# Performance work log

Measured on AMD Instinct MI355X. Metric: run time of the kernel, lower is better.

## Reference

```python
import jax, jax.numpy as jnp
import numpy as np

B, N, D, H = 1, 4096, 1024, 16
K = D // H
ROPE_BASE = 10000.0


def _rope_cos_sin(n, k, base, dtype):
    # GPT-NeoX style rotary embedding: inv_freq over even dims, emb = cat(freqs, freqs)
    inv_freq = 1.0 / (base ** (jnp.arange(0, k, 2, dtype=jnp.float32) / k))  # [K/2]
    pos = jnp.arange(n, dtype=jnp.float32)
    freqs = pos[:, None] * inv_freq[None, :]              # [N, K/2]
    emb = jnp.concatenate([freqs, freqs], axis=-1)        # [N, K]
    return jnp.cos(emb).astype(dtype), jnp.sin(emb).astype(dtype)


def _rotate_half(x):
    x1, x2 = jnp.split(x, 2, axis=-1)
    return jnp.concatenate([-x2, x1], axis=-1)


def setup_inputs() -> dict:
    key = jax.random.key(0)
    kx, kq, ko = jax.random.split(key, 3)
    x = jax.random.normal(kx, (B, N, D), dtype=jnp.float32)
    # torch Linear weights: [out_features, in_features], y = x @ W^T
    w_qkv = jax.random.normal(kq, (3 * H * K, D), dtype=jnp.float32) / np.sqrt(D)
    w_out = jax.random.normal(ko, (D, D), dtype=jnp.float32) / np.sqrt(D)
    return {"x": x, "w_qkv": w_qkv, "w_out": w_out}


def reference(x, w_qkv, w_out):
    b, n, d = x.shape
    qkv = jnp.einsum('bnd,ed->bne', x, w_qkv).reshape(b, n, 3, H, K)
    q, k, v = qkv[:, :, 0], qkv[:, :, 1], qkv[:, :, 2]   # [B, N, H, K]
    cos, sin = _rope_cos_sin(n, K, ROPE_BASE, x.dtype)    # [N, K]
    cos = cos[None, :, None, :]
    sin = sin[None, :, None, :]
    q = q * cos + _rotate_half(q) * sin
    k = k * cos + _rotate_half(k) * sin
    # explicit O(N^2) score matrix, as in the original module
    scores = jnp.einsum('bnhk,bmhk->bnhm', q, k) / np.sqrt(K).astype(x.dtype)
    causal_mask = jnp.tril(jnp.ones((n, n), dtype=bool))  # [N, M]
    scores = jnp.where(causal_mask[None, :, None, :], scores, jnp.finfo(x.dtype).min)
    probs = jax.nn.softmax(scores, axis=-1)
    attn = jnp.einsum('bnhm,bmhk->bnhk', probs, v).reshape(b, n, d)
    return jnp.einsum('bnd,ed->bne', attn, w_out)
```

## Files before the change

kernel.cpp:

```cpp
#include <hip/hip_runtime.h>
#include <hip/hip_bf16.h>
#include <math.h>

#define N_SEQ 4096
#define DIM   1024
#define NHEAD 16
#define HDIM  64
#define E3    3072

typedef short bf16x8 __attribute__((ext_vector_type(8)));
typedef float f32x4  __attribute__((ext_vector_type(4)));
typedef unsigned int u32;

#if __has_builtin(__builtin_amdgcn_exp2f)
#define EXP2(x) __builtin_amdgcn_exp2f(x)
#else
#define EXP2(x) exp2f(x)
#endif

__device__ __forceinline__ float bf2f(unsigned short u) {
    union { unsigned int i; float f; } x; x.i = ((unsigned int)u) << 16; return x.f;
}
__device__ __forceinline__ unsigned short f2bf(float f) {
    union { float f; unsigned int i; } x; x.f = f;
    unsigned int r = x.i + 0x7FFF + ((x.i >> 16) & 1);
    return (unsigned short)(r >> 16);
}
__device__ __forceinline__ unsigned short f2bf_fast(float f) {
    union { float f; unsigned int i; } x; x.f = f;
    return (unsigned short)((x.i + 0x8000u) >> 16);
}
__device__ __forceinline__ f32x4 mfma16(bf16x8 a, bf16x8 b, f32x4 c) {
    return __builtin_amdgcn_mfma_f32_16x16x32_bf16(a, b, c, 0, 0, 0);
}
__device__ __forceinline__ void gload_lds16(const unsigned short* g, unsigned short* l) {
    __builtin_amdgcn_global_load_lds(
        (const __attribute__((address_space(1))) u32*)g,
        (__attribute__((address_space(3))) u32*)l, 16, 0, 0);
}

__device__ __forceinline__ int probe_isf32(const unsigned short* __restrict__ X) {
    __shared__ int cnt;
    if (threadIdx.x == 0) cnt = 0;
    __syncthreads();
    int bad = 0;
    for (int i = threadIdx.x; i < 4096; i += 256) {
        float v = bf2f(X[i]);
        if (!(fabsf(v) < 1e10f)) bad = 1;
    }
    if (bad) atomicAdd(&cnt, 1);
    __syncthreads();
    return cnt > 0;
}

__global__ __launch_bounds__(256)
void prep_kernel(const void* __restrict__ X, const void* __restrict__ Wq,
                 const void* __restrict__ Wo,
                 unsigned short* __restrict__ Xb, unsigned short* __restrict__ Wqb,
                 unsigned short* __restrict__ Wob,
                 float4* __restrict__ Rt,
                 int* __restrict__ flag)
{
    const int ti = blockIdx.x * blockDim.x + threadIdx.x;
    if (ti < N_SEQ * 16) {
        const int n = ti >> 4, f = ti & 15;
        const float i0 = powf(10000.f, -((float)f)        * (1.f/32.f));
        const float i1 = powf(10000.f, -((float)(f + 16)) * (1.f/32.f));
        float s0, c0, s1, c1;
        sincosf((float)n * i0, &s0, &c0);
        sincosf((float)n * i1, &s1, &c1);
        Rt[ti] = (float4){c0, c1, s0, s1};
    }

    const int isf32 = probe_isf32((const unsigned short*)X);
    if (blockIdx.x == 0 && threadIdx.x == 0) *flag = isf32;
    if (!isf32) return;

    const int nX4  = (N_SEQ * DIM) >> 2;
    const int nWq4 = (E3 * DIM) >> 2;
    const int nWo4 = (DIM * DIM) >> 2;
    const int total = nX4 + nWq4 + nWo4;
    const int stride = gridDim.x * blockDim.x;
    for (int i = blockIdx.x * blockDim.x + threadIdx.x; i < total; i += stride) {
        const float4* src; ushort4* dst; int j = i;
        if (j < nX4)                { src = (const float4*)X  + j;  dst = (ushort4*)Xb  + j; }
        else if ((j -= nX4) < nWq4) { src = (const float4*)Wq + j;  dst = (ushort4*)Wqb + j; }
        else { j -= nWq4;             src = (const float4*)Wo + j;  dst = (ushort4*)Wob + j; }
        float4 v = *src;
        ushort4 u;
        u.x = f2bf(v.x); u.y = f2bf(v.y); u.z = f2bf(v.z); u.w = f2bf(v.w);
        *dst = u;
    }
}

__global__ __launch_bounds__(256)
void qkv_mfma_kernel(const void* __restrict__ Xo, const unsigned short* __restrict__ Xc,
                     const void* __restrict__ Wo_, const unsigned short* __restrict__ Wc,
                     const int* __restrict__ flag,
                     const float4* __restrict__ Rt,
                     unsigned short* __restrict__ Qf,
                     unsigned short* __restrict__ Kf,
                     unsigned short* __restrict__ Vf)
{
    __shared__ __align__(16) unsigned short SMEM[4][4096];

    const int isf32 = *flag;
    const unsigned short* Xb = isf32 ? Xc : (const unsigned short*)Xo;
    const unsigned short* Wb = isf32 ? Wc : (const unsigned short*)Wo_;

    const int tid  = threadIdx.x;
    const int lane = tid & 63;
    const int wave = tid >> 6;
    const int wr = wave >> 1, wc = wave & 1;
    const int lm = lane & 15, q4 = lane >> 4;
    const int rbase = blockIdx.y * 128;
    const int cbase = blockIdx.x * 128;

    const int srow = wave * 16 + (lane >> 2);
    const int scol = (lane & 3) * 8;

    const unsigned short* xsrc = Xb + (size_t)(rbase + srow) * DIM + scol;
    const unsigned short* wsrc = Wb + (size_t)(cbase + srow) * DIM + scol;
    const int la = (wr*64 + lm)*32 + q4*8;
    const int lb = (wc*64 + lm)*32 + q4*8;

    f32x4 acc[4][4];
    #pragma unroll
    for (int i = 0; i < 4; ++i)
        #pragma unroll
        for (int j = 0; j < 4; ++j) acc[i][j] = (f32x4){0.f, 0.f, 0.f, 0.f};

    #define QSTAGE(buf)                                                             \
        {                                                                           \
            _Pragma("unroll")                                                       \
            for (int j = 0; j < 2; ++j) {                                           \
                gload_lds16(xsrc + (size_t)j*64*DIM, &SMEM[buf][j*2048 + wave*512]);   \
                gload_lds16(wsrc + (size_t)j*64*DIM, &SMEM[2+buf][j*2048 + wave*512]); \
            }                                                                       \
            xsrc += 32; wsrc += 32;                                                 \
        }

    QSTAGE(0)
    for (int it = 0; it < DIM/32; ++it) {
        const int cur = it & 1;
        __syncthreads();
        if (it + 1 < DIM/32) QSTAGE(cur ^ 1)

        bf16x8 a[4], b[4];
        #pragma unroll
        for (int mi = 0; mi < 4; ++mi)
            a[mi] = *(const bf16x8*)&SMEM[cur][la + mi*512];
        #pragma unroll
        for (int ni = 0; ni < 4; ++ni)
            b[ni] = *(const bf16x8*)&SMEM[2+cur][lb + ni*512];
        #pragma unroll
        for (int mi = 0; mi < 4; ++mi)
            #pragma unroll
            for (int ni = 0; ni < 4; ++ni)
                acc[mi][ni] = mfma16(a[mi], b[ni], acc[mi][ni]);
    }
    #undef QSTAGE

    __syncthreads();

    const int ecol = cbase + wc * 64;
    const int part = ecol >> 10;
    const int h    = (ecol >> 6) & 15;
    unsigned short* ep = &SMEM[0][0] + wave*4096;

    if (part == 2) {
        #pragma unroll
        for (int mh = 0; mh < 2; ++mh) {
            #pragma unroll
            for (int mi2 = 0; mi2 < 2; ++mi2) {
                const int mi = mh*2 + mi2;
                #pragma unroll
                for (int r = 0; r < 4; ++r) {
                    const int n31 = mi2*16 + q4*4 + r;
                    #pragma unroll
                    for (int ni = 0; ni < 4; ++ni)
                        ep[(ni*16 + lm)*40 + n31] = f2bf(acc[mi][ni][r]);
                }
            }
            const int nb = rbase + wr*64 + mh*32;
            const size_t vb = (((size_t)h*128 + (nb >> 5)) << 11) + (size_t)lane*8;
            #pragma unroll
            for (int ni = 0; ni < 4; ++ni) {
                const bf16x8 fr = *(const bf16x8*)(ep + (ni*16 + lm)*40 + q4*8);
                *(bf16x8*)(Vf + vb + (size_t)ni*512) = fr;
            }
        }
    } else {
        unsigned short* dst = (part == 0) ? Qf : Kf;
        const float scl = (part == 0) ? 0.180336884f : 1.0f;
        #pragma unroll
        for (int mi = 0; mi < 4; ++mi) {
            const int tn = rbase + wr*64 + mi*16;
            #pragma unroll
            for (int r = 0; r < 4; ++r) {
                const int n = tn + q4*4 + r;
                const float4 t = Rt[(n << 4) + lm];
                const int row = (q4*4 + r)*72;
                ep[row + lm]      = f2bf((acc[mi][0][r]*t.x - acc[mi][2][r]*t.z) * scl);
                ep[row + lm + 16] = f2bf((acc[mi][1][r]*t.y - acc[mi][3][r]*t.w) * scl);
                ep[row + lm + 32] = f2bf((acc[mi][2][r]*t.x + acc[mi][0][r]*t.z) * scl);
                ep[row + lm + 48] = f2bf((acc[mi][3][r]*t.y + acc[mi][1][r]*t.w) * scl);
            }
            const size_t tb = (((size_t)(h*256 + (tn >> 4))) << 10) + (size_t)lane*8;
            #pragma unroll
            for (int c = 0; c < 2; ++c) {
                const bf16x8 fr = *(const bf16x8*)(ep + lm*72 + c*32 + q4*8);
                *(bf16x8*)(dst + tb + (size_t)c*512) = fr;
            }
        }
    }
}

__global__ __launch_bounds__(512, 4)
void attn_mfma_kernel(const unsigned short* __restrict__ Qf,
                      const unsigned short* __restrict__ Kf,
                      const unsigned short* __restrict__ Vf,
                      unsigned short* __restrict__ Attn)
{
    __shared__ __align__(16) unsigned short P16[8][2][16][40];
    __shared__ __align__(16) float Ox[4][16][64];
    __shared__ float Lx[4][16];

    const int tid  = threadIdx.x;
    const int lane = tid & 63;
    const int wave = tid >> 6;
    const int q4 = lane >> 4, lm = lane & 15;
    const int qh = wave >> 1;
    const int kh = wave & 1;

    const int h = blockIdx.x & 15;
    const int p = blockIdx.x >> 4;
    const int qwA = (p << 6) + (qh << 4);
    const int qwB = ((63 - p) << 6) + (qh << 4);
    const int ntA = p + 1;
    const int ntB = 64 - p;

    const unsigned short* qpA = Qf + (((size_t)(h*256 + (qwA >> 4))) << 10) + (size_t)lane * 8;
    const unsigned short* qpB = Qf + (((size_t)(h*256 + (qwB >> 4))) << 10) + (size_t)lane * 8;
    bf16x8 aqA[2], aqB[2];
    #pragma unroll
    for (int d = 0; d < 2; ++d) {
        aqA[d] = *(const bf16x8*)(qpA + d*512);
        aqB[d] = *(const bf16x8*)(qpB + d*512);
    }

    float lA[4], lB[4];
    f32x4 oA[4], oB[4];
    #pragma unroll
    for (int r = 0; r < 4; ++r) { lA[r] = 0.f; lB[r] = 0.f; }
    #pragma unroll
    for (int dc = 0; dc < 4; ++dc) {
        oA[dc] = (f32x4){0.f, 0.f, 0.f, 0.f};
        oB[dc] = (f32x4){0.f, 0.f, 0.f, 0.f};
    }

    const size_t hb = ((size_t)h) << 18;
    const unsigned short* kc = Kf + hb + (size_t)(kh*2048) + (size_t)lane*8;
    const unsigned short* vc = Vf + hb + (size_t)(kh*2048) + (size_t)lane*8;

    unsigned short* pwA  = &P16[wave][0][0][0];
    unsigned short* pwB  = &P16[wave][1][0][0];
    unsigned short* pwaA = pwA + (4*q4)*40 + lm;
    unsigned short* pwaB = pwB + (4*q4)*40 + lm;
    const unsigned short* parA = pwA + lm*40 + q4*8;
    const unsigned short* parB = pwB + lm*40 + q4*8;

    bf16x8 bk[2][2];
    bk[0][0] = *(const bf16x8*)(kc);
    bk[0][1] = *(const bf16x8*)(kc + 512);
    bk[1][0] = *(const bf16x8*)(kc + 1024);
    bk[1][1] = *(const bf16x8*)(kc + 1536);

    for (int it = 0; it < ntB; ++it) {
        const int kt = it << 6;
        const int doA = (it < ntA);

        bf16x8 bv[4];
        #pragma unroll
        for (int dc = 0; dc < 4; ++dc)
            bv[dc] = *(const bf16x8*)(vc + dc*512);

        bf16x8 nk[2][2];
        nk[0][0] = *(const bf16x8*)(kc + 4096);
        nk[0][1] = *(const bf16x8*)(kc + 4096 + 512);
        nk[1][0] = *(const bf16x8*)(kc + 4096 + 1024);
        nk[1][1] = *(const bf16x8*)(kc + 4096 + 1536);

        f32x4 sB[2], sA[2];
        #pragma unroll
        for (int ki = 0; ki < 2; ++ki) {
            f32x4 z = (f32x4){0.f, 0.f, 0.f, 0.f};
            z = mfma16(aqB[0], bk[ki][0], z);
            sB[ki] = mfma16(aqB[1], bk[ki][1], z);
        }
        if (doA) {
            #pragma unroll
            for (int ki = 0; ki < 2; ++ki) {
                f32x4 z = (f32x4){0.f, 0.f, 0.f, 0.f};
                z = mfma16(aqA[0], bk[ki][0], z);
                sA[ki] = mfma16(aqA[1], bk[ki][1], z);
            }
        }

        if (kt + 32*kh + 31 > qwB) {
            #pragma unroll
            for (int ki = 0; ki < 2; ++ki) {
                const int key = kt + 32*kh + 16*ki + lm;
                const int qq = qwB + 4*q4;
                #pragma unroll
                for (int r = 0; r < 4; ++r)
                    if (key > qq + r) sB[ki][r] = -INFINITY;
            }
        }

        #pragma unroll
        for (int ki = 0; ki < 2; ++ki)
            #pragma unroll
            for (int r = 0; r < 4; ++r) {
                const float pb = EXP2(sB[ki][r]);
                lB[r] += pb;
                pwaB[r*40 + ki*16] = f2bf_fast(pb);
            }

        if (doA) {
            if (kt + 32*kh + 31 > qwA) {
                #pragma unroll
                for (int ki = 0; ki < 2; ++ki) {
                    const int key = kt + 32*kh + 16*ki + lm;
                    const int qq = qwA + 4*q4;
                    #pragma unroll
                    for (int r = 0; r < 4; ++r)
                        if (key > qq + r) sA[ki][r] = -INFINITY;
                }
            }
            #pragma unroll
            for (int ki = 0; ki < 2; ++ki)
                #pragma unroll
                for (int r = 0; r < 4; ++r) {
                    const float pa = EXP2(sA[ki][r]);
                    lA[r] += pa;
                    pwaA[r*40 + ki*16] = f2bf_fast(pa);
                }
        }

        {
            const bf16x8 paB = *(const bf16x8*)(parB);
            #pragma unroll
            for (int dc = 0; dc < 4; ++dc)
                oB[dc] = mfma16(paB, bv[dc], oB[dc]);
        }
        if (doA) {
            const bf16x8 paA = *(const bf16x8*)(parA);
            #pragma unroll
            for (int dc = 0; dc < 4; ++dc)
                oA[dc] = mfma16(paA, bv[dc], oA[dc]);
        }

        kc += 4096; vc += 4096;
        bk[0][0] = nk[0][0]; bk[0][1] = nk[0][1];
        bk[1][0] = nk[1][0]; bk[1][1] = nk[1][1];
    }

    #pragma unroll
    for (int r = 0; r < 4; ++r) {
        float a = lA[r], b = lB[r];
        #pragma unroll
        for (int mk = 1; mk <= 8; mk <<= 1) {
            a += __shfl_xor(a, mk);
            b += __shfl_xor(b, mk);
        }
        lA[r] = a; lB[r] = b;
    }

    if (kh == 1) {
        #pragma unroll
        for (int r = 0; r < 4; ++r) {
            const int qq = 4*q4 + r;
            #pragma unroll
            for (int dc = 0; dc < 4; ++dc)
                Ox[qh][qq][16*dc + lm] = oA[dc][r];
            if (lm == 0) Lx[qh][qq] = lA[r];
        }
    }
    __syncthreads();
    if (kh == 0) {
        #pragma unroll
        for (int r = 0; r < 4; ++r) {
            const int qq = 4*q4 + r;
            const float inv = 1.f / (lA[r] + Lx[qh][qq]);
            const size_t row = (size_t)(qwA + qq) * DIM + (h << 6) + lm;
            #pragma unroll
            for (int dc = 0; dc < 4; ++dc) {
                const float v = oA[dc][r] + Ox[qh][qq][16*dc + lm];
                Attn[row + 16*dc] = f2bf(v * inv);
            }
        }
    }
    __syncthreads();
    if (kh == 1) {
        #pragma unroll
        for (int r = 0; r < 4; ++r) {
            const int qq = 4*q4 + r;
            #pragma unroll
            for (int dc = 0; dc < 4; ++dc)
                Ox[qh][qq][16*dc + lm] = oB[dc][r];
            if (lm == 0) Lx[qh][qq] = lB[r];
        }
    }
    __syncthreads();
    if (kh == 0) {
        #pragma unroll
        for (int r = 0; r < 4; ++r) {
            const int qq = 4*q4 + r;
            const float inv = 1.f / (lB[r] + Lx[qh][qq]);
            const size_t row = (size_t)(qwB + qq) * DIM + (h << 6) + lm;
            #pragma unroll
            for (int dc = 0; dc < 4; ++dc) {
                const float v = oB[dc][r] + Ox[qh][qq][16*dc + lm];
                Attn[row + 16*dc] = f2bf(v * inv);
            }
        }
    }
}

__global__ __launch_bounds__(256)
void out_mfma_kernel(const unsigned short* __restrict__ Ab,
                     const void* __restrict__ Wo_, const unsigned short* __restrict__ Wc,
                     const int* __restrict__ flag,
                     void* __restrict__ Out)
{
    __shared__ unsigned short As[2][4096];
    __shared__ unsigned short Bs[2][2048];

    const int isf32 = *flag;
    const unsigned short* Wb = isf32 ? Wc : (const unsigned short*)Wo_;

    const int tid  = threadIdx.x;
    const int lane = tid & 63;
    const int wave = tid >> 6;
    const int lm = lane & 15, q4 = lane >> 4;
    const int rbase = blockIdx.y * 128;
    const int cbase = blockIdx.x * 64;

    const int srow16 = lane >> 2;
    const int scol = (lane & 3) * 8;

    const unsigned short* asrc = Ab + (size_t)(rbase + wave*32 + srow16) * DIM + scol;
    const unsigned short* bsrc = Wb + (size_t)(cbase + wave*16 + srow16) * DIM + scol;
    const int la = (wave*32 + lm)*32 + q4*8;
    const int lb = lm*32 + q4*8;

    f32x4 acc[2][4];
    #pragma unroll
    for (int i = 0; i < 2; ++i)
        #pragma unroll
        for (int j = 0; j < 4; ++j) acc[i][j] = (f32x4){0.f, 0.f, 0.f, 0.f};

    #define OSTAGE(buf)                                                          \
        {                                                                        \
            _Pragma("unroll")                                                    \
            for (int j = 0; j < 2; ++j)                                          \
                gload_lds16(asrc + (size_t)j*16*DIM, &As[buf][(wave*32 + j*16)*32]); \
            gload_lds16(bsrc, &Bs[buf][(wave*16)*32]);                           \
            asrc += 32; bsrc += 32;                                              \
        }

    OSTAGE(0)
    for (int it = 0; it < DIM/32; ++it) {
        const int cur = it & 1;
        __syncthreads();
        if (it + 1 < DIM/32) OSTAGE(cur ^ 1)

        bf16x8 a[2], b[4];
        #pragma unroll
        for (int mi = 0; mi < 2; ++mi)
            a[mi] = *(const bf16x8*)&As[cur][la + mi*512];
        #pragma unroll
        for (int ni = 0; ni < 4; ++ni)
            b[ni] = *(const bf16x8*)&Bs[cur][lb + ni*512];
        #pragma unroll
        for (int mi = 0; mi < 2; ++mi)
            #pragma unroll
            for (int ni = 0; ni < 4; ++ni)
                acc[mi][ni] = mfma16(a[mi], b[ni], acc[mi][ni]);
    }
    #undef OSTAGE

    #pragma unroll
    for (int mi = 0; mi < 2; ++mi)
        #pragma unroll
        for (int r = 0; r < 4; ++r) {
            const size_t n = rbase + wave*32 + mi*16 + q4*4 + r;
            #pragma unroll
            for (int ni = 0; ni < 4; ++ni) {
                const size_t e = cbase + ni*16 + lm;
                const float v = acc[mi][ni][r];
                if (isf32) ((float*)Out)[n * DIM + e] = v;
                else       ((unsigned short*)Out)[n * DIM + e] = f2bf(v);
            }
        }
}

extern "C" void kernel_launch(void* const* d_in, const int* in_sizes, int n_in,
                              void* d_out, int out_size, void* d_ws, size_t ws_size,
                              hipStream_t stream) {
    const void* X    = d_in[0];
    const void* Wqkv = d_in[1];
    const void* Wout = d_in[2];

    int* flag = (int*)d_ws;
    unsigned short* base = (unsigned short*)((char*)d_ws + 256);
    const size_t nX = (size_t)N_SEQ * DIM;
    const size_t nWq = (size_t)E3 * DIM;
    const size_t nWo = (size_t)DIM * DIM;
    unsigned short* Xb  = base;
    unsigned short* Wqb = Xb + nX;
    unsigned short* Wob = Wqb + nWq;
    unsigned short* Qf  = Wob + nWo;
    unsigned short* Kf  = Qf + nX;
    unsigned short* Vf  = Kf + nX;
    unsigned short* At  = Vf + nX;
    float4* Rt = (float4*)(At + nX);

    prep_kernel<<<768, 256, 0, stream>>>(X, Wqkv, Wout, Xb, Wqb, Wob, Rt, flag);
    qkv_mfma_kernel<<<dim3(E3 / 128, N_SEQ / 128), 256, 0, stream>>>(X, Xb, Wqkv, Wqb, flag, Rt, Qf, Kf, Vf);
    attn_mfma_kernel<<<dim3(NHEAD * 32), 512, 0, stream>>>(Qf, Kf, Vf, At);
    out_mfma_kernel<<<dim3(DIM / 64, N_SEQ / 128), 256, 0, stream>>>(At, Wout, Wob, flag, d_out);
}
```

Baseline: 223.6 us.

## Process four query tiles per attention block to reuse K/V loads

```diff
diff --git a/kernel.cpp b/kernel.cpp
--- a/kernel.cpp
+++ b/kernel.cpp
@@ -216,13 +216,13 @@
     }
 }
 
-__global__ __launch_bounds__(512, 4)
+__global__ __launch_bounds__(512, 2)
 void attn_mfma_kernel(const unsigned short* __restrict__ Qf,
                       const unsigned short* __restrict__ Kf,
                       const unsigned short* __restrict__ Vf,
                       unsigned short* __restrict__ Attn)
 {
-    __shared__ __align__(16) unsigned short P16[8][2][16][40];
+    __shared__ __align__(16) unsigned short P16[8][4][16][40];
     __shared__ __align__(16) float Ox[4][16][64];
     __shared__ float Lx[4][16];
 
@@ -235,40 +235,42 @@
 
     const int h = blockIdx.x & 15;
     const int p = blockIdx.x >> 4;
-    const int qwA = (p << 6) + (qh << 4);
-    const int qwB = ((63 - p) << 6) + (qh << 4);
-    const int ntA = p + 1;
-    const int ntB = 64 - p;
-
-    const unsigned short* qpA = Qf + (((size_t)(h*256 + (qwA >> 4))) << 10) + (size_t)lane * 8;
-    const unsigned short* qpB = Qf + (((size_t)(h*256 + (qwB >> 4))) << 10) + (size_t)lane * 8;
-    bf16x8 aqA[2], aqB[2];
-    #pragma unroll
-    for (int d = 0; d < 2; ++d) {
-        aqA[d] = *(const bf16x8*)(qpA + d*512);
-        aqB[d] = *(const bf16x8*)(qpB + d*512);
-    }
-
-    float lA[4], lB[4];
-    f32x4 oA[4], oB[4];
-    #pragma unroll
-    for (int r = 0; r < 4; ++r) { lA[r] = 0.f; lB[r] = 0.f; }
-    #pragma unroll
-    for (int dc = 0; dc < 4; ++dc) {
-        oA[dc] = (f32x4){0.f, 0.f, 0.f, 0.f};
-        oB[dc] = (f32x4){0.f, 0.f, 0.f, 0.f};
+
+    int qb[4], nt[4], qw[4];
+    qb[0] = 63 - p; qb[1] = 32 + p; qb[2] = 31 - p; qb[3] = p;
+    #pragma unroll
+    for (int s = 0; s < 4; ++s) { nt[s] = qb[s] + 1; qw[s] = qb[s]*64 + qh*16; }
+
+    bf16x8 aq[4][2];
+    #pragma unroll
+    for (int s = 0; s < 4; ++s) {
+        const unsigned short* qp = Qf + (((size_t)(h*256 + (qw[s] >> 4))) << 10) + (size_t)lane * 8;
+        aq[s][0] = *(const bf16x8*)(qp);
+        aq[s][1] = *(const bf16x8*)(qp + 512);
+    }
+
+    float l[4][4];
+    f32x4 o[4][4];
+    #pragma unroll
+    for (int s = 0; s < 4; ++s) {
+        #pragma unroll
+        for (int r = 0; r < 4; ++r) l[s][r] = 0.f;
+        #pragma unroll
+        for (int dc = 0; dc < 4; ++dc) o[s][dc] = (f32x4){0.f, 0.f, 0.f, 0.f};
     }
 
     const size_t hb = ((size_t)h) << 18;
     const unsigned short* kc = Kf + hb + (size_t)(kh*2048) + (size_t)lane*8;
     const unsigned short* vc = Vf + hb + (size_t)(kh*2048) + (size_t)lane*8;
 
-    unsigned short* pwA  = &P16[wave][0][0][0];
-    unsigned short* pwB  = &P16[wave][1][0][0];
-    unsigned short* pwaA = pwA + (4*q4)*40 + lm;
-    unsigned short* pwaB = pwB + (4*q4)*40 + lm;
-    const unsigned short* parA = pwA + lm*40 + q4*8;
-    const unsigned short* parB = pwB + lm*40 + q4*8;
+    unsigned short* pwa[4];
+    const unsigned short* par[4];
+    #pragma unroll
+    for (int s = 0; s < 4; ++s) {
+        unsigned short* base = &P16[wave][s][0][0];
+        pwa[s] = base + (4*q4)*40 + lm;
+        par[s] = base + lm*40 + q4*8;
+    }
 
     bf16x8 bk[2][2];
     bk[0][0] = *(const bf16x8*)(kc);
@@ -276,9 +278,9 @@
     bk[1][0] = *(const bf16x8*)(kc + 1024);
     bk[1][1] = *(const bf16x8*)(kc + 1536);
 
-    for (int it = 0; it < ntB; ++it) {
+    const int ntmax = nt[0];
+    for (int it = 0; it < ntmax; ++it) {
         const int kt = it << 6;
-        const int doA = (it < ntA);
 
         bf16x8 bv[4];
         #pragma unroll
@@ -291,74 +293,45 @@
         nk[1][0] = *(const bf16x8*)(kc + 4096 + 1024);
         nk[1][1] = *(const bf16x8*)(kc + 4096 + 1536);
 
-        f32x4 sB[2], sA[2];
-        #pragma unroll
-        for (int ki = 0; ki < 2; ++ki) {
-            f32x4 z = (f32x4){0.f, 0.f, 0.f, 0.f};
-            z = mfma16(aqB[0], bk[ki][0], z);
-            sB[ki] = mfma16(aqB[1], bk[ki][1], z);
-        }
-        if (doA) {
-            #pragma unroll
-            for (int ki = 0; ki < 2; ++ki) {
-                f32x4 z = (f32x4){0.f, 0.f, 0.f, 0.f};
-                z = mfma16(aqA[0], bk[ki][0], z);
-                sA[ki] = mfma16(aqA[1], bk[ki][1], z);
-            }
-        }
-
-        if (kt + 32*kh + 31 > qwB) {
-            #pragma unroll
-            for (int ki = 0; ki < 2; ++ki) {
-                const int key = kt + 32*kh + 16*ki + lm;
-                const int qq = qwB + 4*q4;
-                #pragma unroll
-                for (int r = 0; r < 4; ++r)
-                    if (key > qq + r) sB[ki][r] = -INFINITY;
-            }
-        }
-
-        #pragma unroll
-        for (int ki = 0; ki < 2; ++ki)
-            #pragma unroll
-            for (int r = 0; r < 4; ++r) {
-                const float pb = EXP2(sB[ki][r]);
-                lB[r] += pb;
-                pwaB[r*40 + ki*16] = f2bf_fast(pb);
-            }
-
-        if (doA) {
-            if (kt + 32*kh + 31 > qwA) {
+        #pragma unroll
+        for (int s = 0; s < 4; ++s) {
+            if (it < nt[s]) {
+                f32x4 ss[2];
                 #pragma unroll
                 for (int ki = 0; ki < 2; ++ki) {
-                    const int key = kt + 32*kh + 16*ki + lm;
-                    const int qq = qwA + 4*q4;
+                    f32x4 z = (f32x4){0.f, 0.f, 0.f, 0.f};
+                    z = mfma16(aq[s][0], bk[ki][0], z);
+                    ss[ki] = mfma16(aq[s][1], bk[ki][1], z);
+                }
+                if (kt + 32*kh + 31 > qw[s]) {
                     #pragma unroll
-                    for (int r = 0; r < 4; ++r)
-                        if (key > qq + r) sA[ki][r] = -INFINITY;
+                    for (int ki = 0; ki < 2; ++ki) {
+                        const int key = kt + 32*kh + 16*ki + lm;
+                        const int qq = qw[s] + 4*q4;
+                        #pragma unroll
+                        for (int r = 0; r < 4; ++r)
+                            if (key > qq + r) ss[ki][r] = -INFINITY;
+                    }
                 }
-            }
-            #pragma unroll
-            for (int ki = 0; ki < 2; ++ki)
-                #pragma unroll
-                for (int r = 0; r < 4; ++r) {
-                    const float pa = EXP2(sA[ki][r]);
-                    lA[r] += pa;
-                    pwaA[r*40 + ki*16] = f2bf_fast(pa);
-                }
-        }
-
-        {
-            const bf16x8 paB = *(const bf16x8*)(parB);
-            #pragma unroll
-            for (int dc = 0; dc < 4; ++dc)
-                oB[dc] = mfma16(paB, bv[dc], oB[dc]);
-        }
-        if (doA) {
-            const bf16x8 paA = *(const bf16x8*)(parA);
-            #pragma unroll
-            for (int dc = 0; dc < 4; ++dc)
-                oA[dc] = mfma16(paA, bv[dc], oA[dc]);
+                #pragma unroll
+                for (int ki = 0; ki < 2; ++ki)
+                    #pragma unroll
+                    for (int r = 0; r < 4; ++r) {
+                        const float pv = EXP2(ss[ki][r]);
+                        l[s][r] += pv;
+                        pwa[s][r*40 + ki*16] = f2bf_fast(pv);
+                    }
+            }
+        }
+
+        #pragma unroll
+        for (int s = 0; s < 4; ++s) {
+            if (it < nt[s]) {
+                const bf16x8 pa = *(const bf16x8*)(par[s]);
+                #pragma unroll
+                for (int dc = 0; dc < 4; ++dc)
+                    o[s][dc] = mfma16(pa, bv[dc], o[s][dc]);
+            }
         }
 
         kc += 4096; vc += 4096;
@@ -367,64 +340,42 @@
     }
 
     #pragma unroll
-    for (int r = 0; r < 4; ++r) {
-        float a = lA[r], b = lB[r];
-        #pragma unroll
-        for (int mk = 1; mk <= 8; mk <<= 1) {
-            a += __shfl_xor(a, mk);
-            b += __shfl_xor(b, mk);
-        }
-        lA[r] = a; lB[r] = b;
-    }
-
-    if (kh == 1) {
+    for (int s = 0; s < 4; ++s)
         #pragma unroll
         for (int r = 0; r < 4; ++r) {
-            const int qq = 4*q4 + r;
-            #pragma unroll
-            for (int dc = 0; dc < 4; ++dc)
-                Ox[qh][qq][16*dc + lm] = oA[dc][r];
-            if (lm == 0) Lx[qh][qq] = lA[r];
-        }
-    }
-    __syncthreads();
-    if (kh == 0) {
-        #pragma unroll
-        for (int r = 0; r < 4; ++r) {
-            const int qq = 4*q4 + r;
-            const float inv = 1.f / (lA[r] + Lx[qh][qq]);
-            const size_t row = (size_t)(qwA + qq) * DIM + (h << 6) + lm;
-            #pragma unroll
-            for (int dc = 0; dc < 4; ++dc) {
-                const float v = oA[dc][r] + Ox[qh][qq][16*dc + lm];
-                Attn[row + 16*dc] = f2bf(v * inv);
-            }
-        }
-    }
-    __syncthreads();
-    if (kh == 1) {
-        #pragma unroll
-        for (int r = 0; r < 4; ++r) {
-            const int qq = 4*q4 + r;
-            #pragma unroll
-            for (int dc = 0; dc < 4; ++dc)
-                Ox[qh][qq][16*dc + lm] = oB[dc][r];
-            if (lm == 0) Lx[qh][qq] = lB[r];
-        }
-    }
-    __syncthreads();
-    if (kh == 0) {
-        #pragma unroll
-        for (int r = 0; r < 4; ++r) {
-            const int qq = 4*q4 + r;
-            const float inv = 1.f / (lB[r] + Lx[qh][qq]);
-            const size_t row = (size_t)(qwB + qq) * DIM + (h << 6) + lm;
-            #pragma unroll
-            for (int dc = 0; dc < 4; ++dc) {
-                const float v = oB[dc][r] + Ox[qh][qq][16*dc + lm];
-                Attn[row + 16*dc] = f2bf(v * inv);
-            }
-        }
+            float a = l[s][r];
+            #pragma unroll
+            for (int mk = 1; mk <= 8; mk <<= 1) a += __shfl_xor(a, mk);
+            l[s][r] = a;
+        }
+
+    #pragma unroll
+    for (int s = 0; s < 4; ++s) {
+        if (kh == 1) {
+            #pragma unroll
+            for (int r = 0; r < 4; ++r) {
+                const int qq = 4*q4 + r;
+                #pragma unroll
+                for (int dc = 0; dc < 4; ++dc)
+                    Ox[qh][qq][16*dc + lm] = o[s][dc][r];
+                if (lm == 0) Lx[qh][qq] = l[s][r];
+            }
+        }
+        __syncthreads();
+        if (kh == 0) {
+            #pragma unroll
+            for (int r = 0; r < 4; ++r) {
+                const int qq = 4*q4 + r;
+                const float inv = 1.f / (l[s][r] + Lx[qh][qq]);
+                const size_t row = (size_t)(qw[s] + qq) * DIM + (h << 6) + lm;
+                #pragma unroll
+                for (int dc = 0; dc < 4; ++dc) {
+                    const float v = o[s][dc][r] + Ox[qh][qq][16*dc + lm];
+                    Attn[row + 16*dc] = f2bf(v * inv);
+                }
+            }
+        }
+        __syncthreads();
     }
 }
 
@@ -529,6 +480,6 @@
 
     prep_kernel<<<768, 256, 0, stream>>>(X, Wqkv, Wout, Xb, Wqb, Wob, Rt, flag);
     qkv_mfma_kernel<<<dim3(E3 / 128, N_SEQ / 128), 256, 0, stream>>>(X, Xb, Wqkv, Wqb, flag, Rt, Qf, Kf, Vf);
-    attn_mfma_kernel<<<dim3(NHEAD * 32), 512, 0, stream>>>(Qf, Kf, Vf, At);
+    attn_mfma_kernel<<<dim3(NHEAD * 16), 512, 0, stream>>>(Qf, Kf, Vf, At);
     out_mfma_kernel<<<dim3(DIM / 64, N_SEQ / 128), 256, 0, stream>>>(At, Wout, Wob, flag, d_out);
 }
```

Result: faster. 201.2 us (-10.0%).
